# Optimization experiments

Hardware: AMD Instinct MI355X
Metric: run time of the kernel (lower is better)

## Reference

```python
import jax, jax.numpy as jnp
import numpy as np

EPS = 1e-6
H = 12  # heads

def layernorm(x, alpha, bias):
    # Faithful to source: unbiased std (ddof=1) and division by (std + eps)
    mean = jnp.mean(x, axis=-1, keepdims=True)
    std = jnp.std(x, axis=-1, ddof=1, keepdims=True)
    return alpha * (x - mean) / (std + EPS) + bias

def setup_inputs() -> dict:
    key = jax.random.key(0)
    ks = jax.random.split(key, 8)
    B, S, D, F = 2, 2048, 768, 3072
    w_scale = 0.02  # keep activations in a sane range
    return {
        "x": jax.random.normal(ks[0], (B, S, D), dtype=jnp.float32),
        "src_mask": jnp.ones((B, 1, 1, S), dtype=jnp.int32),
        "wq": jax.random.normal(ks[1], (D, D), dtype=jnp.float32) * w_scale,
        "wk": jax.random.normal(ks[2], (D, D), dtype=jnp.float32) * w_scale,
        "wv": jax.random.normal(ks[3], (D, D), dtype=jnp.float32) * w_scale,
        "wo": jax.random.normal(ks[4], (D, D), dtype=jnp.float32) * w_scale,
        "w1": jax.random.normal(ks[5], (D, F), dtype=jnp.float32) * w_scale,
        "b1": jnp.zeros((F,), dtype=jnp.float32),
        "w2": jax.random.normal(ks[6], (F, D), dtype=jnp.float32) * w_scale,
        "b2": jnp.zeros((D,), dtype=jnp.float32),
        "ln1_alpha": jnp.ones((1,), dtype=jnp.float32),
        "ln1_bias": jnp.zeros((1,), dtype=jnp.float32),
        "ln2_alpha": jnp.ones((1,), dtype=jnp.float32),
        "ln2_bias": jnp.zeros((1,), dtype=jnp.float32),
    }

def reference(x, src_mask, wq, wk, wv, wo, w1, b1, w2, b2,
              ln1_alpha, ln1_bias, ln2_alpha, ln2_bias):
    B, S, D = x.shape
    dk = D // H
    # ---- residual 1: pre-LN self-attention ----
    t = layernorm(x, ln1_alpha, ln1_bias)
    q = (t @ wq).reshape(B, S, H, dk).transpose(0, 2, 1, 3)  # [B,H,S,dk]
    k = (t @ wk).reshape(B, S, H, dk).transpose(0, 2, 1, 3)
    v = (t @ wv).reshape(B, S, H, dk).transpose(0, 2, 1, 3)
    scores = jnp.einsum('bhqd,bhkd->bhqk', q, k) / jnp.sqrt(jnp.float32(dk))
    # Faithful to source quirk: masked positions are SET to 1e-9 (not -inf)
    scores = jnp.where(src_mask == 0, jnp.float32(1e-9), scores)
    attn = jax.nn.softmax(scores, axis=-1)
    o = jnp.einsum('bhqk,bhkd->bhqd', attn, v)
    o = o.transpose(0, 2, 1, 3).reshape(B, S, D) @ wo
    x = x + o
    # ---- residual 2: pre-LN FFN ----
    t = layernorm(x, ln2_alpha, ln2_bias)
    ffn = jax.nn.relu(t @ w1 + b1) @ w2 + b2
    return x + ffn
```

## Files before the change

### kernel.cpp

```cpp
#include <hip/hip_runtime.h>

#define AS1 __attribute__((address_space(1)))
#define AS3 __attribute__((address_space(3)))

typedef float f32x4 __attribute__((ext_vector_type(4)));
typedef __bf16 bf16x8 __attribute__((ext_vector_type(8)));

__device__ __forceinline__ unsigned short f2bf(float f) {
    union { float f; unsigned u; } v; v.f = f;
    unsigned r = v.u + 0x7fffu + ((v.u >> 16) & 1u);
    return (unsigned short)(r >> 16);
}

__device__ __forceinline__ void async16(const void* g, void* l) {
    __builtin_amdgcn_global_load_lds((AS1 void*)g, (AS3 void*)l, 16, 0, 0);
}

#define SWZ4(r) ((((r) & 3) ^ (((r) >> 2) & 3)))

__global__ void transpose_cvt(const float* __restrict__ W, unsigned short* __restrict__ Wt,
                              int K, int N) {
    __shared__ float tile[32][33];
    int n0 = blockIdx.x * 32, k0 = blockIdx.y * 32;
    int tx = threadIdx.x, ty = threadIdx.y;
#pragma unroll
    for (int i = 0; i < 32; i += 8)
        tile[ty + i][tx] = W[(size_t)(k0 + ty + i) * N + n0 + tx];
    __syncthreads();
#pragma unroll
    for (int i = 0; i < 32; i += 8)
        Wt[(size_t)(n0 + ty + i) * K + k0 + tx] = f2bf(tile[tx][ty + i]);
}

__global__ __launch_bounds__(256) void ln_kernel(const float* __restrict__ x,
                                                 unsigned short* __restrict__ t,
                                                 const float* __restrict__ alpha,
                                                 const float* __restrict__ bias) {
    const int row = blockIdx.x;
    const float* xr = x + (size_t)row * 768;
    float v[3], sum = 0.f, ss = 0.f;
#pragma unroll
    for (int i = 0; i < 3; i++) {
        v[i] = xr[threadIdx.x + 256 * i];
        sum += v[i]; ss += v[i] * v[i];
    }
#pragma unroll
    for (int off = 32; off; off >>= 1) {
        sum += __shfl_down(sum, off);
        ss  += __shfl_down(ss, off);
    }
    __shared__ float s1[4], s2[4];
    int wid = threadIdx.x >> 6, lane = threadIdx.x & 63;
    if (lane == 0) { s1[wid] = sum; s2[wid] = ss; }
    __syncthreads();
    if (threadIdx.x == 0) {
        float a = 0.f, b = 0.f;
#pragma unroll
        for (int i = 0; i < 4; i++) { a += s1[i]; b += s2[i]; }
        s1[0] = a; s2[0] = b;
    }
    __syncthreads();
    sum = s1[0]; ss = s2[0];
    float mean = sum * (1.f / 768.f);
    float var = (ss - sum * mean) * (1.f / 767.f);
    float sc = alpha[0] / (sqrtf(fmaxf(var, 0.f)) + 1e-6f);
    float bs = bias[0];
#pragma unroll
    for (int i = 0; i < 3; i++)
        t[(size_t)row * 768 + threadIdx.x + 256 * i] = f2bf(sc * (v[i] - mean) + bs);
}

template <int MODE>
__global__ __launch_bounds__(256, 2) void gemm_bt(
    const unsigned short* __restrict__ A, const unsigned short* __restrict__ Bt,
    int M, int N, int K, const float* __restrict__ bias,
    const float* __restrict__ res, void* __restrict__ outp) {
    __shared__ __align__(16) unsigned short As[128 * 32];
    __shared__ __align__(16) unsigned short Bs[128 * 32];
    const int tid = threadIdx.x;
    const int lane = tid & 63, w = tid >> 6;
    const int wm = w & 1, wn = w >> 1;
    const int m0 = blockIdx.y * 128, n0 = blockIdx.x * 128;
    const int quad = lane >> 4, l16 = lane & 15;

    const int s0 = (2 * w) * 64 + lane;
    const int r0 = s0 >> 2, g0 = s0 & 3;
    const int s1 = s0 + 64;
    const int r1 = s1 >> 2, g1 = s1 & 3;
    const unsigned short* gA0 = A  + (size_t)(m0 + r0) * K + ((g0 ^ SWZ4(r0)) * 8);
    const unsigned short* gA1 = A  + (size_t)(m0 + r1) * K + ((g1 ^ SWZ4(r1)) * 8);
    const unsigned short* gB0 = Bt + (size_t)(n0 + r0) * K + ((g0 ^ SWZ4(r0)) * 8);
    const unsigned short* gB1 = Bt + (size_t)(n0 + r1) * K + ((g1 ^ SWZ4(r1)) * 8);
    unsigned short* lA0 = As + (2 * w) * 512;
    unsigned short* lA1 = As + (2 * w + 1) * 512;
    unsigned short* lB0 = Bs + (2 * w) * 512;
    unsigned short* lB1 = Bs + (2 * w + 1) * 512;

    f32x4 acc[4][4];
    const f32x4 z = {0.f, 0.f, 0.f, 0.f};
#pragma unroll
    for (int mt = 0; mt < 4; mt++)
#pragma unroll
        for (int nt = 0; nt < 4; nt++) acc[mt][nt] = z;

    const int nK = K >> 5;
    for (int kt = 0; kt < nK; ++kt) {
        __syncthreads();
        async16(gA0, lA0); async16(gA1, lA1);
        async16(gB0, lB0); async16(gB1, lB1);
        gA0 += 32; gA1 += 32; gB0 += 32; gB1 += 32;
        __syncthreads();
        bf16x8 af[4], bf[4];
#pragma unroll
        for (int mt = 0; mt < 4; mt++) {
            int r = 64 * wm + 16 * mt + l16;
            af[mt] = *(const bf16x8*)&As[r * 32 + ((quad ^ SWZ4(r)) * 8)];
        }
#pragma unroll
        for (int nt = 0; nt < 4; nt++) {
            int r = 64 * wn + 16 * nt + l16;
            bf[nt] = *(const bf16x8*)&Bs[r * 32 + ((quad ^ SWZ4(r)) * 8)];
        }
#pragma unroll
        for (int mt = 0; mt < 4; mt++)
#pragma unroll
            for (int nt = 0; nt < 4; nt++)
                acc[mt][nt] = __builtin_amdgcn_mfma_f32_16x16x32_bf16(af[mt], bf[nt], acc[mt][nt], 0, 0, 0);
    }

#pragma unroll
    for (int mt = 0; mt < 4; mt++) {
#pragma unroll
        for (int nt = 0; nt < 4; nt++) {
            const int col = n0 + 64 * wn + 16 * nt + l16;
            float bv = 0.f;
            if (MODE == 1 || MODE == 3) bv = bias[col];
#pragma unroll
            for (int r = 0; r < 4; r++) {
                const int row = m0 + 64 * wm + 16 * mt + quad * 4 + r;
                const size_t idx = (size_t)row * N + col;
                const float v = acc[mt][nt][r];
                if (MODE == 0) ((unsigned short*)outp)[idx] = f2bf(v);
                else if (MODE == 1) ((unsigned short*)outp)[idx] = f2bf(fmaxf(v + bv, 0.f));
                else if (MODE == 2) ((float*)outp)[idx] = v + res[idx];
                else ((float*)outp)[idx] = v + bv + res[idx];
            }
        }
    }
}

__global__ void v_transpose(const unsigned short* __restrict__ qkvc,
                            unsigned short* __restrict__ vt) {
    __shared__ unsigned short t[64][65];
    const int bh = blockIdx.y, b = bh / 12, h = bh % 12;
    const int s0 = blockIdx.x * 64;
    const int tx = threadIdx.x, ty = threadIdx.y;
#pragma unroll
    for (int i = 0; i < 64; i += 4)
        t[ty + i][tx] = qkvc[(size_t)(b * 2048 + s0 + ty + i) * 2304 + 1536 + h * 64 + tx];
    __syncthreads();
#pragma unroll
    for (int i = 0; i < 64; i += 4)
        vt[((size_t)bh * 64 + ty + i) * 2048 + s0 + tx] = t[tx][ty + i];
}

__global__ __launch_bounds__(256, 3) void flash_attn(
    const unsigned short* __restrict__ qkvc,
    const unsigned short* __restrict__ vt,
    const int* __restrict__ mask,
    unsigned short* __restrict__ attno) {
    const int bh = blockIdx.y, b = bh / 12, h = bh % 12;
    const int s0 = blockIdx.x * 64;
    __shared__ __align__(16) unsigned short UQP[4 * 16 * 136];
    __shared__ __align__(16) unsigned short Ks[128 * 64];
    __shared__ __align__(16) unsigned short Vs[64 * 128];
    __shared__ int Ms[128];
    const int tid = threadIdx.x, lane = tid & 63, w = tid >> 6;
    const int quad = lane >> 4, l16 = lane & 15;

    {
        int sl0 = (2 * w) * 64 + lane;
        int r0 = sl0 >> 3, g0 = sl0 & 7;
        int sl1 = sl0 + 64;
        int r1 = sl1 >> 3, g1 = sl1 & 7;
        async16(qkvc + (size_t)(b * 2048 + s0 + r0) * 2304 + h * 64 + ((g0 ^ (r0 & 7)) * 8),
                UQP + (2 * w) * 512);
        async16(qkvc + (size_t)(b * 2048 + s0 + r1) * 2304 + h * 64 + ((g1 ^ (r1 & 7)) * 8),
                UQP + (2 * w + 1) * 512);
    }
    __syncthreads();
    bf16x8 aQ[2];
    {
        int r = 16 * w + l16;
#pragma unroll
        for (int kk = 0; kk < 2; kk++)
            aQ[kk] = *(const bf16x8*)&UQP[r * 64 + (((kk * 4 + quad) ^ (r & 7)) * 8)];
    }
    __bf16* Ps = (__bf16*)(UQP + w * (16 * 136));

    f32x4 Oacc[4], Lacc;
    const f32x4 z = {0.f, 0.f, 0.f, 0.f};
#pragma unroll
    for (int nt = 0; nt < 4; nt++) Oacc[nt] = z;
    Lacc = z;
    bf16x8 ones;
#pragma unroll
    for (int i = 0; i < 8; i++) ones[i] = (__bf16)1.0f;

    const unsigned short* kbase = qkvc + 768;
    const unsigned short* vbase = vt + (size_t)bh * 64 * 2048;
    const float SCL = 0.125f * 1.44269504088896340736f;
    const float MSK = 1.4426950408889634e-9f;

    for (int j = 0; j < 16; j++) {
        const int k0 = j * 128;
        __syncthreads();
#pragma unroll
        for (int c = 0; c < 4; c++) {
            int sl = (4 * w + c) * 64 + lane;
            int r = sl >> 3, g = sl & 7;
            async16(kbase + (size_t)(b * 2048 + k0 + r) * 2304 + h * 64 + ((g ^ (r & 7)) * 8),
                    Ks + (4 * w + c) * 512);
        }
#pragma unroll
        for (int c = 0; c < 4; c++) {
            int sl = (4 * w + c) * 64 + lane;
            int r = sl >> 4, g = sl & 15;
            async16(vbase + (size_t)r * 2048 + k0 + ((g ^ (r & 15)) * 8),
                    Vs + (4 * w + c) * 512);
        }
        if (tid < 128) Ms[tid] = mask[b * 2048 + k0 + tid];
        __syncthreads();

        f32x4 sc[8];
#pragma unroll
        for (int nt = 0; nt < 8; nt++) {
            int rr = nt * 16 + l16;
            bf16x8 bk0 = *(const bf16x8*)&Ks[rr * 64 + (((0 + quad) ^ (rr & 7)) * 8)];
            bf16x8 bk1 = *(const bf16x8*)&Ks[rr * 64 + (((4 + quad) ^ (rr & 7)) * 8)];
            sc[nt] = __builtin_amdgcn_mfma_f32_16x16x32_bf16(aQ[0], bk0, z, 0, 0, 0);
            sc[nt] = __builtin_amdgcn_mfma_f32_16x16x32_bf16(aQ[1], bk1, sc[nt], 0, 0, 0);
        }
#pragma unroll
        for (int nt = 0; nt < 8; nt++) {
            const int msk = Ms[nt * 16 + l16];
#pragma unroll
            for (int r = 0; r < 4; r++) {
                float v = msk ? sc[nt][r] * SCL : MSK;
                sc[nt][r] = __builtin_amdgcn_exp2f(v);
            }
        }
#pragma unroll
        for (int nt = 0; nt < 8; nt++)
#pragma unroll
            for (int r = 0; r < 4; r++)
                Ps[(quad * 4 + r) * 136 + nt * 16 + l16] = (__bf16)sc[nt][r];

#pragma unroll
        for (int ktile = 0; ktile < 4; ktile++) {
            bf16x8 aP = *(const bf16x8*)&Ps[l16 * 136 + ktile * 32 + quad * 8];
            Lacc = __builtin_amdgcn_mfma_f32_16x16x32_bf16(aP, ones, Lacc, 0, 0, 0);
#pragma unroll
            for (int nt = 0; nt < 4; nt++) {
                int rr = nt * 16 + l16;
                bf16x8 bv = *(const bf16x8*)&Vs[rr * 128 + (((ktile * 4 + quad) ^ (rr & 15)) * 8)];
                Oacc[nt] = __builtin_amdgcn_mfma_f32_16x16x32_bf16(aP, bv, Oacc[nt], 0, 0, 0);
            }
        }
    }

    float inv[4];
#pragma unroll
    for (int r = 0; r < 4; r++) inv[r] = 1.0f / Lacc[r];
#pragma unroll
    for (int nt = 0; nt < 4; nt++)
#pragma unroll
        for (int r = 0; r < 4; r++) {
            const int row = s0 + 16 * w + quad * 4 + r;
            attno[(size_t)(b * 2048 + row) * 768 + h * 64 + nt * 16 + l16] =
                f2bf(Oacc[nt][r] * inv[r]);
        }
}

extern "C" void kernel_launch(void* const* d_in, const int* in_sizes, int n_in,
                              void* d_out, int out_size, void* d_ws, size_t ws_size,
                              hipStream_t stream) {
    const float* x    = (const float*)d_in[0];
    const int*   mask = (const int*)d_in[1];
    const float* wq   = (const float*)d_in[2];
    const float* wk   = (const float*)d_in[3];
    const float* wv   = (const float*)d_in[4];
    const float* wo   = (const float*)d_in[5];
    const float* w1   = (const float*)d_in[6];
    const float* b1   = (const float*)d_in[7];
    const float* w2   = (const float*)d_in[8];
    const float* b2   = (const float*)d_in[9];
    const float* ln1a = (const float*)d_in[10];
    const float* ln1b = (const float*)d_in[11];
    const float* ln2a = (const float*)d_in[12];
    const float* ln2b = (const float*)d_in[13];

    char* p = (char*)d_ws;
    auto carve = [&](size_t bytes) {
        char* q = p;
        p += (bytes + 255) & ~(size_t)255;
        return q;
    };
    unsigned short* wTqkv = (unsigned short*)carve((size_t)2304 * 768 * 2);
    unsigned short* wTo   = (unsigned short*)carve((size_t)768 * 768 * 2);
    unsigned short* wT1   = (unsigned short*)carve((size_t)3072 * 768 * 2);
    unsigned short* wT2   = (unsigned short*)carve((size_t)768 * 3072 * 2);
    unsigned short* vtb   = (unsigned short*)carve((size_t)24 * 64 * 2048 * 2);
    float*          x1    = (float*)carve((size_t)4096 * 768 * 4);
    char* unionA = carve((size_t)4096 * 768 * 2 + (size_t)4096 * 2304 * 2);
    unsigned short* t1   = (unsigned short*)unionA;
    unsigned short* qkvc = (unsigned short*)(unionA + (size_t)4096 * 768 * 2);
    unsigned short* ffnh = (unsigned short*)unionA;
    unsigned short* attno = (unsigned short*)carve((size_t)4096 * 768 * 2);
    unsigned short* t2 = attno;

    dim3 tb(32, 8);
    transpose_cvt<<<dim3(24, 24), tb, 0, stream>>>(wq, wTqkv, 768, 768);
    transpose_cvt<<<dim3(24, 24), tb, 0, stream>>>(wk, wTqkv + (size_t)768 * 768, 768, 768);
    transpose_cvt<<<dim3(24, 24), tb, 0, stream>>>(wv, wTqkv + (size_t)1536 * 768, 768, 768);
    transpose_cvt<<<dim3(24, 24), tb, 0, stream>>>(wo, wTo, 768, 768);
    transpose_cvt<<<dim3(96, 24), tb, 0, stream>>>(w1, wT1, 768, 3072);
    transpose_cvt<<<dim3(24, 96), tb, 0, stream>>>(w2, wT2, 3072, 768);

    ln_kernel<<<4096, 256, 0, stream>>>(x, t1, ln1a, ln1b);
    gemm_bt<0><<<dim3(18, 32), 256, 0, stream>>>(t1, wTqkv, 4096, 2304, 768,
                                                 nullptr, nullptr, qkvc);
    v_transpose<<<dim3(32, 24), dim3(64, 4), 0, stream>>>(qkvc, vtb);
    flash_attn<<<dim3(32, 24), 256, 0, stream>>>(qkvc, vtb, mask, attno);
    gemm_bt<2><<<dim3(6, 32), 256, 0, stream>>>(attno, wTo, 4096, 768, 768,
                                                nullptr, x, x1);
    ln_kernel<<<4096, 256, 0, stream>>>(x1, t2, ln2a, ln2b);
    gemm_bt<1><<<dim3(24, 32), 256, 0, stream>>>(t2, wT1, 4096, 3072, 768,
                                                 b1, nullptr, ffnh);
    gemm_bt<3><<<dim3(6, 32), 256, 0, stream>>>(ffnh, wT2, 4096, 768, 3072,
                                                b2, x1, (float*)d_out);
}
```

Before: 321.0 us.

## Add 64x64-tile GEMM kernel for N=768 projections to fill more CUs

```diff
diff --git a/kernel.cpp b/kernel.cpp
--- a/kernel.cpp
+++ b/kernel.cpp
@@ -145,6 +145,64 @@
                 else if (MODE == 2) ((float*)outp)[idx] = v + res[idx];
                 else ((float*)outp)[idx] = v + bv + res[idx];
             }
+        }
+    }
+}
+
+template <int MODE>
+__global__ __launch_bounds__(256, 3) void gemm64_bt(
+    const unsigned short* __restrict__ A, const unsigned short* __restrict__ Bt,
+    int M, int N, int K, const float* __restrict__ bias,
+    const float* __restrict__ res, void* __restrict__ outp) {
+    __shared__ __align__(16) unsigned short As[64 * 32];
+    __shared__ __align__(16) unsigned short Bs[64 * 32];
+    const int tid = threadIdx.x;
+    const int lane = tid & 63, w = tid >> 6;
+    const int m0 = blockIdx.y * 64, n0 = blockIdx.x * 64;
+    const int quad = lane >> 4, l16 = lane & 15;
+
+    const int sl = w * 64 + lane;
+    const int r = sl >> 2, g = sl & 3;
+    const unsigned short* gA = A  + (size_t)(m0 + r) * K + ((g ^ SWZ4(r)) * 8);
+    const unsigned short* gB = Bt + (size_t)(n0 + r) * K + ((g ^ SWZ4(r)) * 8);
+    unsigned short* lA = As + w * 512;
+    unsigned short* lB = Bs + w * 512;
+
+    f32x4 acc[4];
+    const f32x4 z = {0.f, 0.f, 0.f, 0.f};
+#pragma unroll
+    for (int nt = 0; nt < 4; nt++) acc[nt] = z;
+
+    const int nK = K >> 5;
+    for (int kt = 0; kt < nK; ++kt) {
+        __syncthreads();
+        async16(gA, lA); async16(gB, lB);
+        gA += 32; gB += 32;
+        __syncthreads();
+        const int ra = 16 * w + l16;
+        bf16x8 af = *(const bf16x8*)&As[ra * 32 + ((quad ^ SWZ4(ra)) * 8)];
+#pragma unroll
+        for (int nt = 0; nt < 4; nt++) {
+            int rb = 16 * nt + l16;
+            bf16x8 bf = *(const bf16x8*)&Bs[rb * 32 + ((quad ^ SWZ4(rb)) * 8)];
+            acc[nt] = __builtin_amdgcn_mfma_f32_16x16x32_bf16(af, bf, acc[nt], 0, 0, 0);
+        }
+    }
+
+#pragma unroll
+    for (int nt = 0; nt < 4; nt++) {
+        const int col = n0 + 16 * nt + l16;
+        float bv = 0.f;
+        if (MODE == 1 || MODE == 3) bv = bias[col];
+#pragma unroll
+        for (int rr = 0; rr < 4; rr++) {
+            const int row = m0 + 16 * w + quad * 4 + rr;
+            const size_t idx = (size_t)row * N + col;
+            const float v = acc[nt][rr];
+            if (MODE == 0) ((unsigned short*)outp)[idx] = f2bf(v);
+            else if (MODE == 1) ((unsigned short*)outp)[idx] = f2bf(fmaxf(v + bv, 0.f));
+            else if (MODE == 2) ((float*)outp)[idx] = v + res[idx];
+            else ((float*)outp)[idx] = v + bv + res[idx];
         }
     }
 }
@@ -332,11 +390,11 @@
                                                  nullptr, nullptr, qkvc);
     v_transpose<<<dim3(32, 24), dim3(64, 4), 0, stream>>>(qkvc, vtb);
     flash_attn<<<dim3(32, 24), 256, 0, stream>>>(qkvc, vtb, mask, attno);
-    gemm_bt<2><<<dim3(6, 32), 256, 0, stream>>>(attno, wTo, 4096, 768, 768,
-                                                nullptr, x, x1);
+    gemm64_bt<2><<<dim3(12, 64), 256, 0, stream>>>(attno, wTo, 4096, 768, 768,
+                                                   nullptr, x, x1);
     ln_kernel<<<4096, 256, 0, stream>>>(x1, t2, ln2a, ln2b);
     gemm_bt<1><<<dim3(24, 32), 256, 0, stream>>>(t2, wT1, 4096, 3072, 768,
                                                  b1, nullptr, ffnh);
-    gemm_bt<3><<<dim3(6, 32), 256, 0, stream>>>(ffnh, wT2, 4096, 768, 3072,
-                                                b2, x1, (float*)d_out);
-}
+    gemm64_bt<3><<<dim3(12, 64), 256, 0, stream>>>(ffnh, wT2, 4096, 768, 3072,
+                                                   b2, x1, (float*)d_out);
+}
```

Result: faster. 306.9 us (-4.4%).
